# Kernel tuning notes

Hardware: AMD Instinct MI355X
Metric: run time of the kernel (lower is better)

The kernel has to match this reference:

```python
import jax, jax.numpy as jnp
import numpy as np

N = 100000   # nodes
E = 1600000  # edges
IN = 128
H = 128
C = 2
EPS = 1e-5   # BatchNorm eps (torch default)


def setup_inputs() -> dict:
    key = jax.random.key(0)
    ks = jax.random.split(key, 40)
    d = {}
    d["x"] = jax.random.normal(ks[0], (N, IN), jnp.float32)
    d["edge_index"] = jax.random.randint(ks[1], (2, E), 0, N, dtype=jnp.int32)
    dims = [(IN, H), (H, H), (H, H), (H, H // 2), (H // 2, C)]
    for i, (a, b) in enumerate(dims):
        d[f"W{i+1}"] = jax.random.normal(ks[2 + 2 * i], (a, b), jnp.float32) / np.float32(np.sqrt(a))
        d[f"b{i+1}"] = jnp.zeros((b,), jnp.float32)
    bdims = [H, H, H, H // 2]
    for i, bd in enumerate(bdims):
        d[f"g{i+1}"] = 1.0 + 0.1 * jax.random.normal(ks[12 + 4 * i], (bd,), jnp.float32)
        d[f"be{i+1}"] = 0.1 * jax.random.normal(ks[13 + 4 * i], (bd,), jnp.float32)
        d[f"rm{i+1}"] = 0.1 * jax.random.normal(ks[14 + 4 * i], (bd,), jnp.float32)
        d[f"rv{i+1}"] = 1.0 + 0.1 * jax.random.uniform(ks[15 + 4 * i], (bd,), jnp.float32)
    return d


def _gcn_conv(x, W, b, src, dst, dinv):
    # PyG GCNConv: h = x @ W; symmetric-norm aggregation with self-loops; + bias
    h = x @ W                                            # [N, out]
    norm = dinv[src] * dinv[dst]                         # [E]
    msg = h[src] * norm[:, None]                         # gather + scale
    agg = jax.ops.segment_sum(msg, dst, num_segments=N)  # scatter-add at dst
    agg = agg + (dinv * dinv)[:, None] * h               # self-loop term
    return agg + b


def _bn_eval(h, g, be, rm, rv):
    # BatchNorm1d in eval mode (running stats)
    return (h - rm) * jax.lax.rsqrt(rv + EPS) * g + be


def reference(x, edge_index,
              W1, b1, W2, b2, W3, b3, W4, b4, W5, b5,
              g1, be1, rm1, rv1, g2, be2, rm2, rv2,
              g3, be3, rm3, rv3, g4, be4, rm4, rv4):
    src, dst = edge_index[0], edge_index[1]
    # degree with self-loops (edge weight 1), computed at destination nodes
    deg = jax.ops.segment_sum(jnp.ones((E,), x.dtype), dst, num_segments=N) + 1.0
    dinv = jax.lax.rsqrt(deg)

    h = jax.nn.relu(_bn_eval(_gcn_conv(x, W1, b1, src, dst, dinv), g1, be1, rm1, rv1))
    h = jax.nn.relu(_bn_eval(_gcn_conv(h, W2, b2, src, dst, dinv), g2, be2, rm2, rv2))
    h = jax.nn.relu(_bn_eval(_gcn_conv(h, W3, b3, src, dst, dinv), g3, be3, rm3, rv3))
    h = jax.nn.relu(_bn_eval(_gcn_conv(h, W4, b4, src, dst, dinv), g4, be4, rm4, rv4))
    return _gcn_conv(h, W5, b5, src, dst, dinv)  # [N, C]
```

## Files before the change

### kernel.cpp

```cpp
#include <hip/hip_runtime.h>
#include <hip/hip_fp16.h>

#define BN_EPS 1e-5f
#define CAP 8192
#define MAXBKT 512

typedef _Float16 half8 __attribute__((ext_vector_type(8)));
typedef float f32x4 __attribute__((ext_vector_type(4)));


__global__ void k_init(int* bucket_cur, int* rowptr, int n, int E) {
    int i = blockIdx.x * blockDim.x + threadIdx.x;
    if (i < MAXBKT) bucket_cur[i] = 0;
    if (i == 0) rowptr[n] = E;
}

__global__ __launch_bounds__(256) void k_bin(const int* __restrict__ src,
        const int* __restrict__ dst, int E, int nbk,
        int* __restrict__ bucket_cur, unsigned* __restrict__ pairs) {
    __shared__ int hist[MAXBKT];
    __shared__ int base_[MAXBKT];
    for (int b = threadIdx.x; b < nbk; b += 256) hist[b] = 0;
    __syncthreads();
    int e0 = blockIdx.x * 2048;
    int my_b[8], my_l[8];
    unsigned my_p[8];
    #pragma unroll
    for (int j = 0; j < 8; j++) {
        int e = e0 + threadIdx.x + j * 256;
        my_b[j] = -1;
        if (e < E) {
            int d = dst[e];
            my_p[j] = (unsigned)src[e] | ((unsigned)(d & 255) << 24);
            my_b[j] = d >> 8;
            my_l[j] = atomicAdd(&hist[my_b[j]], 1);
        }
    }
    __syncthreads();
    for (int b = threadIdx.x; b < nbk; b += 256) {
        int h = hist[b];
        base_[b] = h ? atomicAdd(&bucket_cur[b], h) : 0;
    }
    __syncthreads();
    #pragma unroll
    for (int j = 0; j < 8; j++) {
        if (my_b[j] >= 0) {
            int pos = base_[my_b[j]] + my_l[j];
            if (pos < CAP)
                pairs[(size_t)my_b[j] * CAP + pos] = my_p[j];
        }
    }
}

__global__ __launch_bounds__(256) void k_cntscan(const unsigned* __restrict__ pairs,
        const int* __restrict__ bucket_cur, int* __restrict__ rowptr,
        int* __restrict__ bsums, float* __restrict__ dinv, int n) {
    __shared__ int lc[256];
    __shared__ int tmp[256];
    lc[threadIdx.x] = 0;
    __syncthreads();
    int b = blockIdx.x;
    int m = min(bucket_cur[b], CAP);
    const unsigned* p = pairs + (size_t)b * CAP;
    for (int q = threadIdx.x; q < m; q += 256)
        atomicAdd(&lc[p[q] >> 24], 1);
    __syncthreads();
    int v = lc[threadIdx.x];
    tmp[threadIdx.x] = v;
    __syncthreads();
    for (int off = 1; off < 256; off <<= 1) {
        int t = (threadIdx.x >= off) ? tmp[threadIdx.x - off] : 0;
        __syncthreads();
        tmp[threadIdx.x] += t;
        __syncthreads();
    }
    int node = b * 256 + threadIdx.x;
    if (node < n) {
        rowptr[node] = tmp[threadIdx.x] - v;
        dinv[node] = rsqrtf((float)v + 1.0f);
    }
    if (threadIdx.x == 255) bsums[b] = tmp[255];
}

__global__ void k_scan2(int* bsums, int nb) {
    __shared__ int tmp[1024];
    int v = (threadIdx.x < nb) ? bsums[threadIdx.x] : 0;
    tmp[threadIdx.x] = v;
    __syncthreads();
    for (int off = 1; off < 1024; off <<= 1) {
        int t = (threadIdx.x >= off) ? tmp[threadIdx.x - off] : 0;
        __syncthreads();
        tmp[threadIdx.x] += t;
        __syncthreads();
    }
    if (threadIdx.x < nb) bsums[threadIdx.x] = tmp[threadIdx.x] - v;
}

__global__ void k_scan3(int* __restrict__ rowptr, const int* __restrict__ bsums, int n) {
    int i = blockIdx.x * blockDim.x + threadIdx.x;
    if (i < n) rowptr[i] += bsums[i >> 8];
}

__global__ __launch_bounds__(256) void k_fill2(const unsigned* __restrict__ pairs,
        const int* __restrict__ bucket_cur, const int* __restrict__ rowptr,
        int* __restrict__ csr, int n) {
    __shared__ int cur[256];
    __shared__ int stg[CAP];
    int b = blockIdx.x;
    int node0 = b * 256;
    int nend = min(node0 + 256, n);
    int base_csr = rowptr[node0];
    int node = node0 + threadIdx.x;
    cur[threadIdx.x] = (node < n) ? rowptr[node] - base_csr : 0;
    __syncthreads();
    int m = min(bucket_cur[b], CAP);
    const unsigned* p = pairs + (size_t)b * CAP;
    for (int q = threadIdx.x; q < m; q += 256) {
        unsigned pr = p[q];
        int ofs = atomicAdd(&cur[pr >> 24], 1);
        stg[ofs] = (int)(pr & 0xFFFFFFu);
    }
    __syncthreads();
    int len = rowptr[nend] - base_csr;
    for (int q = threadIdx.x; q < len; q += 256)
        csr[base_csr + q] = stg[q];
}


template<int M>
__global__ void k_wpack(const float* __restrict__ W, half8* __restrict__ Wp) {
    int idx = blockIdx.x * 256 + threadIdx.x;
    constexpr int TOT = (M / 16) * 4 * 64;
    if (idx >= TOT) return;
    int l = idx & 63, tc = idx >> 6;
    int c = tc & 3, t = tc >> 2;
    int g = l >> 4, nn = l & 15;
    int k0 = 32 * c + 8 * g, col = 16 * t + nn;
    half8 hi, lo;
    #pragma unroll
    for (int j = 0; j < 8; j++) {
        float w = W[(size_t)(k0 + j) * M + col];
        _Float16 h = (_Float16)w;
        hi[j] = h;
        lo[j] = (_Float16)(w - (float)h);
    }
    Wp[idx] = hi;
    Wp[TOT + idx] = lo;
}


__device__ __forceinline__ void h8_acc(float* acc, uint4 v) {
    const __half2* p = (const __half2*)&v;
    #pragma unroll
    for (int j = 0; j < 4; j++) {
        float2 f = __half22float2(p[j]);
        acc[2 * j] += f.x;
        acc[2 * j + 1] += f.y;
    }
}


__global__ __launch_bounds__(256) void k_gemm_mfma1(const float* __restrict__ Ain,
        const half8* __restrict__ Wp, const float* __restrict__ dinv,
        __half* __restrict__ out, int n) {
    constexpr int LDR = 136;
    __shared__ _Float16 As[64 * LDR];

    int row0 = blockIdx.x * 64;
    for (int idx = threadIdx.x; idx < 64 * 16; idx += 256) {
        int r = idx >> 4, k2 = idx & 15;
        int grow = row0 + r;
        half8 h = {};
        if (grow < n) {
            float4 va = *(const float4*)&Ain[(size_t)grow * 128 + k2 * 8];
            float4 vb = *(const float4*)&Ain[(size_t)grow * 128 + k2 * 8 + 4];
            h[0] = (_Float16)va.x; h[1] = (_Float16)va.y;
            h[2] = (_Float16)va.z; h[3] = (_Float16)va.w;
            h[4] = (_Float16)vb.x; h[5] = (_Float16)vb.y;
            h[6] = (_Float16)vb.z; h[7] = (_Float16)vb.w;
        }
        *(half8*)&As[r * LDR + k2 * 8] = h;
    }
    __syncthreads();

    int w = threadIdx.x >> 6, l = threadIdx.x & 63;
    int g = l >> 4, nn = l & 15;

    half8 xf[4][4];
    #pragma unroll
    for (int rg = 0; rg < 4; rg++)
        #pragma unroll
        for (int c = 0; c < 4; c++)
            xf[rg][c] = *(const half8*)&As[(16 * rg + nn) * LDR + (4 * c + g) * 8];

    f32x4 acc[4][2];
    #pragma unroll
    for (int rg = 0; rg < 4; rg++)
        #pragma unroll
        for (int tt = 0; tt < 2; tt++)
            acc[rg][tt] = (f32x4){0.f, 0.f, 0.f, 0.f};

    #pragma unroll
    for (int tt = 0; tt < 2; tt++) {
        int t = w * 2 + tt;
        #pragma unroll
        for (int c = 0; c < 4; c++) {
            half8 wh = Wp[(t * 4 + c) * 64 + l];
            half8 wl = Wp[8 * 4 * 64 + (t * 4 + c) * 64 + l];
            #pragma unroll
            for (int rg = 0; rg < 4; rg++) {
                acc[rg][tt] = __builtin_amdgcn_mfma_f32_16x16x32_f16(wh, xf[rg][c], acc[rg][tt], 0, 0, 0);
                acc[rg][tt] = __builtin_amdgcn_mfma_f32_16x16x32_f16(wl, xf[rg][c], acc[rg][tt], 0, 0, 0);
            }
        }
    }

    __syncthreads();
    #pragma unroll
    for (int rg = 0; rg < 4; rg++) {
        int node = row0 + 16 * rg + nn;
        float s = (node < n) ? dinv[node] : 0.f;
        #pragma unroll
        for (int tt = 0; tt < 2; tt++) {
            int colh = 16 * (w * 2 + tt) + 4 * g;
            __half2 p0 = __float22half2_rn(make_float2(acc[rg][tt][0] * s, acc[rg][tt][1] * s));
            __half2 p1 = __float22half2_rn(make_float2(acc[rg][tt][2] * s, acc[rg][tt][3] * s));
            uint2 u;
            u.x = *(unsigned*)&p0;
            u.y = *(unsigned*)&p1;
            *(uint2*)&As[(16 * rg + nn) * LDR + colh] = u;
        }
    }
    __syncthreads();
    for (int idx = threadIdx.x; idx < 64 * 16; idx += 256) {
        int r = idx >> 4, k2 = idx & 15;
        int grow = row0 + r;
        if (grow < n)
            *(uint4*)&out[(size_t)grow * 128 + k2 * 8] = *(const uint4*)&As[r * LDR + k2 * 8];
    }
}


template<int MOUT>
__global__ __launch_bounds__(256) void k_fused_mfma(const __half* __restrict__ ht,
        const int* __restrict__ rowptr, const int* __restrict__ csr,
        const float* __restrict__ dinv, const float* __restrict__ bias,
        const float* __restrict__ gw, const float* __restrict__ bb,
        const float* __restrict__ rm, const float* __restrict__ rv,
        const half8* __restrict__ Wp, __half* __restrict__ out, int n) {
    constexpr int NT = MOUT / 16;
    constexpr int TPW = NT / 4;
    constexpr int LDR = 136;
    __shared__ _Float16 As[64 * LDR];

    int row0 = blockIdx.x * 64;
    int grp = threadIdx.x >> 4;
    int c = threadIdx.x & 15;
    const uint4* h4 = (const uint4*)ht;
    int c0 = c * 8;
    float4 bv0 = *(const float4*)&bias[c0], bv1 = *(const float4*)&bias[c0 + 4];
    float gv[8], bbv[8], rmv[8], rvv[8];
    *(float4*)&gv[0] = *(const float4*)&gw[c0];  *(float4*)&gv[4] = *(const float4*)&gw[c0 + 4];
    *(float4*)&bbv[0] = *(const float4*)&bb[c0]; *(float4*)&bbv[4] = *(const float4*)&bb[c0 + 4];
    *(float4*)&rmv[0] = *(const float4*)&rm[c0]; *(float4*)&rmv[4] = *(const float4*)&rm[c0 + 4];
    *(float4*)&rvv[0] = *(const float4*)&rv[c0]; *(float4*)&rvv[4] = *(const float4*)&rv[c0 + 4];

    for (int p = 0; p < 4; p++) {
        int r = p * 16 + grp;
        int i = row0 + r;
        uint4 u = make_uint4(0, 0, 0, 0);
        if (i < n) {
            float acc[8] = {};
            h8_acc(acc, h4[(size_t)i * 16 + c]);
            int e1 = rowptr[i + 1];
            int e = rowptr[i];
            for (; e + 4 <= e1; e += 4) {
                int s0 = csr[e], s1 = csr[e + 1], s2 = csr[e + 2], s3 = csr[e + 3];
                uint4 v0 = h4[(size_t)s0 * 16 + c];
                uint4 v1 = h4[(size_t)s1 * 16 + c];
                uint4 v2 = h4[(size_t)s2 * 16 + c];
                uint4 v3 = h4[(size_t)s3 * 16 + c];
                h8_acc(acc, v0); h8_acc(acc, v1); h8_acc(acc, v2); h8_acc(acc, v3);
            }
            for (; e < e1; e++)
                h8_acc(acc, h4[(size_t)csr[e] * 16 + c]);
            float di = dinv[i];
            float o[8];
            o[0] = fmaf(acc[0], di, bv0.x); o[1] = fmaf(acc[1], di, bv0.y);
            o[2] = fmaf(acc[2], di, bv0.z); o[3] = fmaf(acc[3], di, bv0.w);
            o[4] = fmaf(acc[4], di, bv1.x); o[5] = fmaf(acc[5], di, bv1.y);
            o[6] = fmaf(acc[6], di, bv1.z); o[7] = fmaf(acc[7], di, bv1.w);
            #pragma unroll
            for (int j = 0; j < 8; j++)
                o[j] = fmaxf(fmaf(o[j] - rmv[j], rsqrtf(rvv[j] + BN_EPS) * gv[j], bbv[j]), 0.f);
            __half2 q0 = __float22half2_rn(make_float2(o[0], o[1]));
            __half2 q1 = __float22half2_rn(make_float2(o[2], o[3]));
            __half2 q2 = __float22half2_rn(make_float2(o[4], o[5]));
            __half2 q3 = __float22half2_rn(make_float2(o[6], o[7]));
            u.x = *(unsigned*)&q0; u.y = *(unsigned*)&q1;
            u.z = *(unsigned*)&q2; u.w = *(unsigned*)&q3;
        }
        *(uint4*)&As[r * LDR + c0] = u;
    }
    __syncthreads();

    int w = threadIdx.x >> 6, l = threadIdx.x & 63;
    int g = l >> 4, nn = l & 15;

    half8 xf[4][4];
    #pragma unroll
    for (int rg = 0; rg < 4; rg++)
        #pragma unroll
        for (int cc = 0; cc < 4; cc++)
            xf[rg][cc] = *(const half8*)&As[(16 * rg + nn) * LDR + (4 * cc + g) * 8];

    f32x4 acc2[4][TPW];
    #pragma unroll
    for (int rg = 0; rg < 4; rg++)
        #pragma unroll
        for (int tt = 0; tt < TPW; tt++)
            acc2[rg][tt] = (f32x4){0.f, 0.f, 0.f, 0.f};

    #pragma unroll
    for (int tt = 0; tt < TPW; tt++) {
        int t = w * TPW + tt;
        #pragma unroll
        for (int cc = 0; cc < 4; cc++) {
            half8 wh = Wp[(t * 4 + cc) * 64 + l];
            half8 wl = Wp[NT * 4 * 64 + (t * 4 + cc) * 64 + l];
            #pragma unroll
            for (int rg = 0; rg < 4; rg++) {
                acc2[rg][tt] = __builtin_amdgcn_mfma_f32_16x16x32_f16(wh, xf[rg][cc], acc2[rg][tt], 0, 0, 0);
                acc2[rg][tt] = __builtin_amdgcn_mfma_f32_16x16x32_f16(wl, xf[rg][cc], acc2[rg][tt], 0, 0, 0);
            }
        }
    }

    __syncthreads();
    #pragma unroll
    for (int rg = 0; rg < 4; rg++) {
        int node = row0 + 16 * rg + nn;
        float s = (node < n) ? dinv[node] : 0.f;
        #pragma unroll
        for (int tt = 0; tt < TPW; tt++) {
            int colh = 16 * (w * TPW + tt) + 4 * g;
            __half2 p0 = __float22half2_rn(make_float2(acc2[rg][tt][0] * s, acc2[rg][tt][1] * s));
            __half2 p1 = __float22half2_rn(make_float2(acc2[rg][tt][2] * s, acc2[rg][tt][3] * s));
            uint2 uu;
            uu.x = *(unsigned*)&p0;
            uu.y = *(unsigned*)&p1;
            *(uint2*)&As[(16 * rg + nn) * LDR + colh] = uu;
        }
    }
    __syncthreads();
    for (int idx = threadIdx.x; idx < 64 * (MOUT / 8); idx += 256) {
        int r = idx / (MOUT / 8), k2 = idx % (MOUT / 8);
        int grow = row0 + r;
        if (grow < n)
            *(uint4*)&out[(size_t)grow * MOUT + k2 * 8] = *(const uint4*)&As[r * LDR + k2 * 8];
    }
}


__global__ __launch_bounds__(256) void k_fused5(const __half* __restrict__ ht,
        const int* __restrict__ rowptr, const int* __restrict__ csr,
        const float* __restrict__ dinv, const float* __restrict__ bias,
        const float* __restrict__ gw, const float* __restrict__ bb,
        const float* __restrict__ rm, const float* __restrict__ rv,
        const float* __restrict__ W5, float* __restrict__ outS, int n) {
    constexpr int LDR = 72;
    __shared__ _Float16 As[64 * LDR];
    __shared__ float Wl[128];
    if (threadIdx.x < 128) Wl[threadIdx.x] = W5[threadIdx.x];

    int row0 = blockIdx.x * 64;
    int grp = threadIdx.x >> 3;
    int c = threadIdx.x & 7;
    const uint4* h4 = (const uint4*)ht;
    int c0 = c * 8;
    float4 bv0 = *(const float4*)&bias[c0], bv1 = *(const float4*)&bias[c0 + 4];
    float gv[8], bbv[8], rmv[8], rvv[8];
    *(float4*)&gv[0] = *(const float4*)&gw[c0];  *(float4*)&gv[4] = *(const float4*)&gw[c0 + 4];
    *(float4*)&bbv[0] = *(const float4*)&bb[c0]; *(float4*)&bbv[4] = *(const float4*)&bb[c0 + 4];
    *(float4*)&rmv[0] = *(const float4*)&rm[c0]; *(float4*)&rmv[4] = *(const float4*)&rm[c0 + 4];
    *(float4*)&rvv[0] = *(const float4*)&rv[c0]; *(float4*)&rvv[4] = *(const float4*)&rv[c0 + 4];

    for (int p = 0; p < 2; p++) {
        int r = p * 32 + grp;
        int i = row0 + r;
        uint4 u = make_uint4(0, 0, 0, 0);
        if (i < n) {
            float acc[8] = {};
            h8_acc(acc, h4[(size_t)i * 8 + c]);
            int e1 = rowptr[i + 1];
            int e = rowptr[i];
            for (; e + 4 <= e1; e += 4) {
                int s0 = csr[e], s1 = csr[e + 1], s2 = csr[e + 2], s3 = csr[e + 3];
                uint4 v0 = h4[(size_t)s0 * 8 + c];
                uint4 v1 = h4[(size_t)s1 * 8 + c];
                uint4 v2 = h4[(size_t)s2 * 8 + c];
                uint4 v3 = h4[(size_t)s3 * 8 + c];
                h8_acc(acc, v0); h8_acc(acc, v1); h8_acc(acc, v2); h8_acc(acc, v3);
            }
            for (; e < e1; e++)
                h8_acc(acc, h4[(size_t)csr[e] * 8 + c]);
            float di = dinv[i];
            float o[8];
            o[0] = fmaf(acc[0], di, bv0.x); o[1] = fmaf(acc[1], di, bv0.y);
            o[2] = fmaf(acc[2], di, bv0.z); o[3] = fmaf(acc[3], di, bv0.w);
            o[4] = fmaf(acc[4], di, bv1.x); o[5] = fmaf(acc[5], di, bv1.y);
            o[6] = fmaf(acc[6], di, bv1.z); o[7] = fmaf(acc[7], di, bv1.w);
            #pragma unroll
            for (int j = 0; j < 8; j++)
                o[j] = fmaxf(fmaf(o[j] - rmv[j], rsqrtf(rvv[j] + BN_EPS) * gv[j], bbv[j]), 0.f);
            __half2 q0 = __float22half2_rn(make_float2(o[0], o[1]));
            __half2 q1 = __float22half2_rn(make_float2(o[2], o[3]));
            __half2 q2 = __float22half2_rn(make_float2(o[4], o[5]));
            __half2 q3 = __float22half2_rn(make_float2(o[6], o[7]));
            u.x = *(unsigned*)&q0; u.y = *(unsigned*)&q1;
            u.z = *(unsigned*)&q2; u.w = *(unsigned*)&q3;
        }
        *(uint4*)&As[r * LDR + c0] = u;
    }
    __syncthreads();

    if (threadIdx.x < 128) {
        int r = threadIdx.x >> 1, cls = threadIdx.x & 1;
        int i = row0 + r;
        if (i < n) {
            float a = 0.f;
            const __half2* row = (const __half2*)&As[r * LDR];
            #pragma unroll
            for (int k2 = 0; k2 < 32; k2++) {
                float2 xx = __half22float2(row[k2]);
                a = fmaf(xx.x, Wl[4 * k2 + cls], a);
                a = fmaf(xx.y, Wl[4 * k2 + 2 + cls], a);
            }
            outS[2 * i + cls] = a * dinv[i];
        }
    }
}


__global__ void k_agg_final(const float* __restrict__ ht, const int* __restrict__ rowptr,
                            const int* __restrict__ csr, const float* __restrict__ dinv,
                            const float* __restrict__ bias, float* __restrict__ out, int n) {
    int i = blockIdx.x * blockDim.x + threadIdx.x;
    if (i >= n) return;
    const float2* h2 = (const float2*)ht;
    float2 t = h2[i];
    float a0 = t.x, a1 = t.y;
    int e1 = rowptr[i + 1];
    int e = rowptr[i];
    for (; e + 4 <= e1; e += 4) {
        int s0 = csr[e], s1 = csr[e + 1], s2 = csr[e + 2], s3 = csr[e + 3];
        float2 u0 = h2[s0], u1 = h2[s1], u2 = h2[s2], u3 = h2[s3];
        a0 += (u0.x + u1.x) + (u2.x + u3.x);
        a1 += (u0.y + u1.y) + (u2.y + u3.y);
    }
    for (; e < e1; e++) {
        float2 u = h2[csr[e]];
        a0 += u.x; a1 += u.y;
    }
    float s = dinv[i];
    out[2 * i]     = fmaf(a0, s, bias[0]);
    out[2 * i + 1] = fmaf(a1, s, bias[1]);
}


extern "C" void kernel_launch(void* const* d_in, const int* in_sizes, int n_in,
                              void* d_out, int out_size, void* d_ws, size_t ws_size,
                              hipStream_t stream) {
    const float* x  = (const float*)d_in[0];
    const int*   ei = (const int*)d_in[1];
    const float* W1 = (const float*)d_in[2];  const float* b1 = (const float*)d_in[3];
    const float* W2 = (const float*)d_in[4];  const float* b2 = (const float*)d_in[5];
    const float* W3 = (const float*)d_in[6];  const float* b3 = (const float*)d_in[7];
    const float* W4 = (const float*)d_in[8];  const float* b4 = (const float*)d_in[9];
    const float* W5 = (const float*)d_in[10]; const float* b5 = (const float*)d_in[11];
    const float* g1 = (const float*)d_in[12]; const float* be1 = (const float*)d_in[13];
    const float* rm1 = (const float*)d_in[14]; const float* rv1 = (const float*)d_in[15];
    const float* g2 = (const float*)d_in[16]; const float* be2 = (const float*)d_in[17];
    const float* rm2 = (const float*)d_in[18]; const float* rv2 = (const float*)d_in[19];
    const float* g3 = (const float*)d_in[20]; const float* be3 = (const float*)d_in[21];
    const float* rm3 = (const float*)d_in[22]; const float* rv3 = (const float*)d_in[23];
    const float* g4 = (const float*)d_in[24]; const float* be4 = (const float*)d_in[25];
    const float* rm4 = (const float*)d_in[26]; const float* rv4 = (const float*)d_in[27];

    const int N = in_sizes[0] / 128;
    const int E = in_sizes[1] / 2;
    const int* src = ei;
    const int* dst = ei + E;
    const int nbk = (N + 255) >> 8;

    char* base = (char*)d_ws;
    size_t off = 0;
    auto carve = [&](size_t bytes) -> void* {
        void* r = base + off;
        off = (off + bytes + 255) & ~(size_t)255;
        return r;
    };
    __half* htA = (__half*)carve((size_t)N * 128 * 2);
    __half* htB = (__half*)carve((size_t)N * 128 * 2);
    float*  htS = (float*)carve((size_t)N * 2 * 4);
    half8*  Wp1 = (half8*)carve(2 * 8 * 4 * 64 * 16);
    half8*  Wp2 = (half8*)carve(2 * 8 * 4 * 64 * 16);
    half8*  Wp3 = (half8*)carve(2 * 8 * 4 * 64 * 16);
    half8*  Wp4 = (half8*)carve(2 * 4 * 4 * 64 * 16);
    unsigned* pairs = (unsigned*)carve((size_t)MAXBKT * CAP * 4);
    int*   bucket_cur = (int*)carve((size_t)MAXBKT * 4);
    int*   rowptr= (int*)carve((size_t)(N + 1) * 4);
    int*   csr   = (int*)carve((size_t)E * 4);
    float* dinv  = (float*)carve((size_t)N * 4);
    int*   bsums = (int*)carve((size_t)nbk * 4);
    (void)ws_size; (void)n_in; (void)out_size;

    float* out = (float*)d_out;

    k_wpack<128><<<8, 256, 0, stream>>>(W1, Wp1);
    k_wpack<128><<<8, 256, 0, stream>>>(W2, Wp2);
    k_wpack<128><<<8, 256, 0, stream>>>(W3, Wp3);
    k_wpack<64><<<4, 256, 0, stream>>>(W4, Wp4);

    k_init   <<<(N + 255) / 256, 256, 0, stream>>>(bucket_cur, rowptr, N, E);
    k_bin    <<<(E + 2047) / 2048, 256, 0, stream>>>(src, dst, E, nbk, bucket_cur, pairs);
    k_cntscan<<<nbk, 256, 0, stream>>>(pairs, bucket_cur, rowptr, bsums, dinv, N);
    k_scan2  <<<1, 1024, 0, stream>>>(bsums, nbk);
    k_scan3  <<<(N + 255) / 256, 256, 0, stream>>>(rowptr, bsums, N);
    k_fill2  <<<nbk, 256, 0, stream>>>(pairs, bucket_cur, rowptr, csr, N);

    const int gb = (N + 63) / 64;
    k_gemm_mfma1<<<gb, 256, 0, stream>>>(x, Wp1, dinv, htA, N);
    k_fused_mfma<128><<<gb, 256, 0, stream>>>(htA, rowptr, csr, dinv, b1, g1, be1, rm1, rv1, Wp2, htB, N);
    k_fused_mfma<128><<<gb, 256, 0, stream>>>(htB, rowptr, csr, dinv, b2, g2, be2, rm2, rv2, Wp3, htA, N);
    k_fused_mfma<64><<<gb, 256, 0, stream>>>(htA, rowptr, csr, dinv, b3, g3, be3, rm3, rv3, Wp4, htB, N);
    k_fused5<<<gb, 256, 0, stream>>>(htB, rowptr, csr, dinv, b4, g4, be4, rm4, rv4, W5, htS, N);
    k_agg_final<<<(N + 255) / 256, 256, 0, stream>>>(htS, rowptr, csr, dinv, b5, out, N);
}
```

Measured before the change: 359.7 us.

## Fuse CSR count/scan/fill into one build kernel and stream CSR indices nontemporally

The CSR build pipeline (count+scan, block-sum scan, scan fixup, fill) is replaced by two kernels. A single-block kernel scans the per-bucket counts, and a per-bucket kernel then computes rowptr, dinv and the CSR fill in one pass. This drops two launches and one re-read of the pairs buffer and rowptr. Separately, the CSR index reads in the aggregation loops become nontemporal loads, so the streamed indices are less likely to evict the gathered feature rows from cache.

```diff
diff --git a/kernel.cpp b/kernel.cpp
--- a/kernel.cpp
+++ b/kernel.cpp
@@ -52,16 +52,33 @@
     }
 }
 
-__global__ __launch_bounds__(256) void k_cntscan(const unsigned* __restrict__ pairs,
-        const int* __restrict__ bucket_cur, int* __restrict__ rowptr,
-        int* __restrict__ bsums, float* __restrict__ dinv, int n) {
+__global__ void k_bsum(const int* __restrict__ bucket_cur, int* __restrict__ bbase, int nbk) {
+    __shared__ int tmp[1024];
+    int v = (threadIdx.x < nbk) ? min(bucket_cur[threadIdx.x], CAP) : 0;
+    tmp[threadIdx.x] = v;
+    __syncthreads();
+    for (int off = 1; off < 1024; off <<= 1) {
+        int t = (threadIdx.x >= off) ? tmp[threadIdx.x - off] : 0;
+        __syncthreads();
+        tmp[threadIdx.x] += t;
+        __syncthreads();
+    }
+    if (threadIdx.x < nbk) bbase[threadIdx.x] = tmp[threadIdx.x] - v;
+}
+
+__global__ __launch_bounds__(256) void k_build(const unsigned* __restrict__ pairs,
+        const int* __restrict__ bucket_cur, const int* __restrict__ bbase,
+        int* __restrict__ rowptr, float* __restrict__ dinv,
+        int* __restrict__ csr, int n) {
     __shared__ int lc[256];
     __shared__ int tmp[256];
-    lc[threadIdx.x] = 0;
-    __syncthreads();
+    __shared__ int cur[256];
+    __shared__ int stg[CAP];
     int b = blockIdx.x;
     int m = min(bucket_cur[b], CAP);
     const unsigned* p = pairs + (size_t)b * CAP;
+    lc[threadIdx.x] = 0;
+    __syncthreads();
     for (int q = threadIdx.x; q < m; q += 256)
         atomicAdd(&lc[p[q] >> 24], 1);
     __syncthreads();
@@ -74,56 +91,23 @@
         tmp[threadIdx.x] += t;
         __syncthreads();
     }
+    int local_excl = tmp[threadIdx.x] - v;
+    int base_b = bbase[b];
     int node = b * 256 + threadIdx.x;
     if (node < n) {
-        rowptr[node] = tmp[threadIdx.x] - v;
+        rowptr[node] = base_b + local_excl;
         dinv[node] = rsqrtf((float)v + 1.0f);
     }
-    if (threadIdx.x == 255) bsums[b] = tmp[255];
-}
-
-__global__ void k_scan2(int* bsums, int nb) {
-    __shared__ int tmp[1024];
-    int v = (threadIdx.x < nb) ? bsums[threadIdx.x] : 0;
-    tmp[threadIdx.x] = v;
-    __syncthreads();
-    for (int off = 1; off < 1024; off <<= 1) {
-        int t = (threadIdx.x >= off) ? tmp[threadIdx.x - off] : 0;
-        __syncthreads();
-        tmp[threadIdx.x] += t;
-        __syncthreads();
-    }
-    if (threadIdx.x < nb) bsums[threadIdx.x] = tmp[threadIdx.x] - v;
-}
-
-__global__ void k_scan3(int* __restrict__ rowptr, const int* __restrict__ bsums, int n) {
-    int i = blockIdx.x * blockDim.x + threadIdx.x;
-    if (i < n) rowptr[i] += bsums[i >> 8];
-}
-
-__global__ __launch_bounds__(256) void k_fill2(const unsigned* __restrict__ pairs,
-        const int* __restrict__ bucket_cur, const int* __restrict__ rowptr,
-        int* __restrict__ csr, int n) {
-    __shared__ int cur[256];
-    __shared__ int stg[CAP];
-    int b = blockIdx.x;
-    int node0 = b * 256;
-    int nend = min(node0 + 256, n);
-    int base_csr = rowptr[node0];
-    int node = node0 + threadIdx.x;
-    cur[threadIdx.x] = (node < n) ? rowptr[node] - base_csr : 0;
-    __syncthreads();
-    int m = min(bucket_cur[b], CAP);
-    const unsigned* p = pairs + (size_t)b * CAP;
+    cur[threadIdx.x] = local_excl;
+    __syncthreads();
     for (int q = threadIdx.x; q < m; q += 256) {
         unsigned pr = p[q];
         int ofs = atomicAdd(&cur[pr >> 24], 1);
         stg[ofs] = (int)(pr & 0xFFFFFFu);
     }
     __syncthreads();
-    int len = rowptr[nend] - base_csr;
-    for (int q = threadIdx.x; q < len; q += 256)
-        csr[base_csr + q] = stg[q];
+    for (int q = threadIdx.x; q < m; q += 256)
+        csr[base_b + q] = stg[q];
 }
 
 
@@ -275,7 +259,10 @@
             int e1 = rowptr[i + 1];
             int e = rowptr[i];
             for (; e + 4 <= e1; e += 4) {
-                int s0 = csr[e], s1 = csr[e + 1], s2 = csr[e + 2], s3 = csr[e + 3];
+                int s0 = __builtin_nontemporal_load(csr + e);
+                int s1 = __builtin_nontemporal_load(csr + e + 1);
+                int s2 = __builtin_nontemporal_load(csr + e + 2);
+                int s3 = __builtin_nontemporal_load(csr + e + 3);
                 uint4 v0 = h4[(size_t)s0 * 16 + c];
                 uint4 v1 = h4[(size_t)s1 * 16 + c];
                 uint4 v2 = h4[(size_t)s2 * 16 + c];
@@ -283,7 +270,7 @@
                 h8_acc(acc, v0); h8_acc(acc, v1); h8_acc(acc, v2); h8_acc(acc, v3);
             }
             for (; e < e1; e++)
-                h8_acc(acc, h4[(size_t)csr[e] * 16 + c]);
+                h8_acc(acc, h4[(size_t)__builtin_nontemporal_load(csr + e) * 16 + c]);
             float di = dinv[i];
             float o[8];
             o[0] = fmaf(acc[0], di, bv0.x); o[1] = fmaf(acc[1], di, bv0.y);
@@ -395,7 +382,10 @@
             int e1 = rowptr[i + 1];
             int e = rowptr[i];
             for (; e + 4 <= e1; e += 4) {
-                int s0 = csr[e], s1 = csr[e + 1], s2 = csr[e + 2], s3 = csr[e + 3];
+                int s0 = __builtin_nontemporal_load(csr + e);
+                int s1 = __builtin_nontemporal_load(csr + e + 1);
+                int s2 = __builtin_nontemporal_load(csr + e + 2);
+                int s3 = __builtin_nontemporal_load(csr + e + 3);
                 uint4 v0 = h4[(size_t)s0 * 8 + c];
                 uint4 v1 = h4[(size_t)s1 * 8 + c];
                 uint4 v2 = h4[(size_t)s2 * 8 + c];
@@ -403,7 +393,7 @@
                 h8_acc(acc, v0); h8_acc(acc, v1); h8_acc(acc, v2); h8_acc(acc, v3);
             }
             for (; e < e1; e++)
-                h8_acc(acc, h4[(size_t)csr[e] * 8 + c]);
+                h8_acc(acc, h4[(size_t)__builtin_nontemporal_load(csr + e) * 8 + c]);
             float di = dinv[i];
             float o[8];
             o[0] = fmaf(acc[0], di, bv0.x); o[1] = fmaf(acc[1], di, bv0.y);
@@ -453,13 +443,16 @@
     int e1 = rowptr[i + 1];
     int e = rowptr[i];
     for (; e + 4 <= e1; e += 4) {
-        int s0 = csr[e], s1 = csr[e + 1], s2 = csr[e + 2], s3 = csr[e + 3];
+        int s0 = __builtin_nontemporal_load(csr + e);
+        int s1 = __builtin_nontemporal_load(csr + e + 1);
+        int s2 = __builtin_nontemporal_load(csr + e + 2);
+        int s3 = __builtin_nontemporal_load(csr + e + 3);
         float2 u0 = h2[s0], u1 = h2[s1], u2 = h2[s2], u3 = h2[s3];
         a0 += (u0.x + u1.x) + (u2.x + u3.x);
         a1 += (u0.y + u1.y) + (u2.y + u3.y);
     }
     for (; e < e1; e++) {
-        float2 u = h2[csr[e]];
+        float2 u = h2[__builtin_nontemporal_load(csr + e)];
         a0 += u.x; a1 += u.y;
     }
     float s = dinv[i];
@@ -509,10 +502,10 @@
     half8*  Wp4 = (half8*)carve(2 * 4 * 4 * 64 * 16);
     unsigned* pairs = (unsigned*)carve((size_t)MAXBKT * CAP * 4);
     int*   bucket_cur = (int*)carve((size_t)MAXBKT * 4);
+    int*   bbase = (int*)carve((size_t)MAXBKT * 4);
     int*   rowptr= (int*)carve((size_t)(N + 1) * 4);
     int*   csr   = (int*)carve((size_t)E * 4);
     float* dinv  = (float*)carve((size_t)N * 4);
-    int*   bsums = (int*)carve((size_t)nbk * 4);
     (void)ws_size; (void)n_in; (void)out_size;
 
     float* out = (float*)d_out;
@@ -522,12 +515,10 @@
     k_wpack<128><<<8, 256, 0, stream>>>(W3, Wp3);
     k_wpack<64><<<4, 256, 0, stream>>>(W4, Wp4);
 
-    k_init   <<<(N + 255) / 256, 256, 0, stream>>>(bucket_cur, rowptr, N, E);
-    k_bin    <<<(E + 2047) / 2048, 256, 0, stream>>>(src, dst, E, nbk, bucket_cur, pairs);
-    k_cntscan<<<nbk, 256, 0, stream>>>(pairs, bucket_cur, rowptr, bsums, dinv, N);
-    k_scan2  <<<1, 1024, 0, stream>>>(bsums, nbk);
-    k_scan3  <<<(N + 255) / 256, 256, 0, stream>>>(rowptr, bsums, N);
-    k_fill2  <<<nbk, 256, 0, stream>>>(pairs, bucket_cur, rowptr, csr, N);
+    k_init <<<(N + 255) / 256, 256, 0, stream>>>(bucket_cur, rowptr, N, E);
+    k_bin  <<<(E + 2047) / 2048, 256, 0, stream>>>(src, dst, E, nbk, bucket_cur, pairs);
+    k_bsum <<<1, 1024, 0, stream>>>(bucket_cur, bbase, nbk);
+    k_build<<<nbk, 256, 0, stream>>>(pairs, bucket_cur, bbase, rowptr, dinv, csr, N);
 
     const int gb = (N + 63) / 64;
     k_gemm_mfma1<<<gb, 256, 0, stream>>>(x, Wp1, dinv, htA, N);
```

After: 397.4 us. 10.5% more time.
